# Optimization experiments

Measured on AMD Instinct MI355X. Metric: run time of the kernel, lower is better.

Reference implementation:

```python
import jax, jax.numpy as jnp
import numpy as np

B, C, K, P, STRIDE, ITERS = 32, 32, 3, 4, 1, 3
PSIZE = P * P
EPS = 1e-6


def unfold_patches(x, K, stride):
    # Replicates F.unfold(x_chw, kernel_size=K, padding=K//2, stride=stride)
    # followed by transpose(1,2).view(b, oh, ow, K*K, c) — including the
    # channel-major flat ordering that the view reinterprets.
    b, h, w, c = x.shape
    pad = K // 2
    xp = jnp.pad(jnp.transpose(x, (0, 3, 1, 2)), ((0, 0), (0, 0), (pad, pad), (pad, pad)))
    oh = (h + 2 * pad - K) // stride + 1
    ow = (w + 2 * pad - K) // stride + 1
    rows = []
    for ki in range(K):
        cols = []
        for kj in range(K):
            cols.append(xp[:, :, ki:ki + (oh - 1) * stride + 1:stride, kj:kj + (ow - 1) * stride + 1:stride])
        rows.append(jnp.stack(cols, axis=2))  # (b, c, K, oh, ow)
    pat = jnp.stack(rows, axis=2)  # (b, c, K, K, oh, ow)
    pat = pat.reshape(b, c * K * K, oh * ow)  # unfold output (b, c*K*K, L)
    pat = jnp.transpose(pat, (0, 2, 1)).reshape(b, oh, ow, K * K, c)
    return pat, oh, ow


def squash(s, eps=EPS):
    s2 = jnp.sum(s * s, axis=-1, keepdims=True)
    return (s2 / (1.0 + s2)) * s / jnp.sqrt(s2 + eps)


def dynamic_routing(v, a_in, iters=ITERS, eps=EPS):
    # v: (n, in_votes, C, psize), a_in: (n, in_votes, 1)
    n, in_votes, Cc, _ = v.shape
    b_ij = jnp.zeros((n, in_votes, Cc), dtype=v.dtype)
    a_in = jnp.clip(a_in, 0.0001, 1.0)
    v_j = None
    for t in range(iters):
        c_ij = jax.nn.softmax(b_ij, axis=2) * a_in
        c_ij = c_ij / (jnp.sum(c_ij, axis=2, keepdims=True) + eps)
        s_j = jnp.einsum('nic,nicq->ncq', c_ij, v)
        v_j = squash(s_j)
        if t < iters - 1:
            agreement = jnp.einsum('nicq,ncq->nic', v, v_j)
            b_ij = b_ij + agreement
    a_out = jnp.clip(jnp.sqrt(jnp.sum(v_j * v_j, axis=-1) + eps), 0.0001, 1.0 - 0.0001)
    return v_j, a_out


def setup_inputs() -> dict:
    key = jax.random.key(0)
    k1, k2 = jax.random.split(key)
    x = jax.random.normal(k1, (2, 14, 14, B * (PSIZE + 1)), dtype=jnp.float32)
    weights = jax.random.normal(k2, (K * K * B, C, PSIZE, PSIZE), dtype=jnp.float32) * 0.02
    return {"x": x, "weights": weights}


def reference(x, weights):
    b, h, w, c = x.shape
    patches, oh, ow = unfold_patches(x, K, STRIDE)
    p_in = patches[..., :B * PSIZE].reshape(b * oh * ow, K * K * B, PSIZE)
    a_in = patches[..., B * PSIZE:].reshape(b * oh * ow, K * K * B, 1)
    votes = jnp.einsum('bip,icpq->bicq', p_in, weights)  # (n, KKB, C, psize)
    p_vec, a_vec = dynamic_routing(votes, a_in)
    p_out = p_vec.reshape(b, oh, ow, C * PSIZE)
    a_out = a_vec.reshape(b, oh, ow, C)
    out = jnp.concatenate([p_out, a_out], axis=3)
    p_out = jnp.nan_to_num(p_out, nan=0.0, posinf=10000.0, neginf=-10000.0)
    a_out = jnp.nan_to_num(a_out, nan=0.5, posinf=1.0 - 0.0001, neginf=0.0001)
    out = jnp.nan_to_num(out, nan=0.0, posinf=10000.0, neginf=-10000.0)
    return p_out, a_out, out
```

## Files before the change

### kernel.cpp

```cpp
#include <hip/hip_runtime.h>
#include <hip/hip_fp16.h>
#include <math.h>

#define NB 392
#define NI 288
#define NC 32
#define NQ 16
#define CQ 512
#define CH 544
#define EPSV 1e-6f

#define VSCALE 32.0f
#define VINV (1.0f / 32.0f)

#define OFF_AOUT 200704
#define OFF_CAT  213248

#define RT_THREADS 512
#define RT_WAVES 8

typedef _Float16 v4h __attribute__((ext_vector_type(4)));
typedef float v4f __attribute__((ext_vector_type(4)));
typedef float v2f __attribute__((ext_vector_type(2)));

__device__ __forceinline__ float gather_x(const float* __restrict__ x, int n, int j) {
    int c_idx = j / 9;
    int rem = j - c_idx * 9;
    int ki = rem / 3;
    int kj = rem - ki * 3;
    int b_ = n / 196;
    int rest = n - b_ * 196;
    int yy = rest / 14;
    int xx = rest - yy * 14;
    int iy = yy + ki - 1;
    int ix = xx + kj - 1;
    float v = 0.f;
    if ((unsigned)iy < 14u && (unsigned)ix < 14u)
        v = x[((b_ * 14 + iy) * 14 + ix) * CH + c_idx];
    return v;
}

__global__ __launch_bounds__(256) void votes_k(const float* __restrict__ x,
                                               const float* __restrict__ wts,
                                               uchar* __restrict__ votes) {
    __shared__ ushort w16l[8192];
    __shared__ uchar tile[64 * 144];
    int mtt = blockIdx.x;
    int i = blockIdx.y;
    int t = threadIdx.x;
    int wv = t >> 6;
    int l = t & 63;
    int col = l & 15;
    int quad = l >> 4;

    {
        const float4* src = (const float4*)(wts + (size_t)i * 8192);
#pragma unroll
        for (int it = 0; it < 8; ++it) {
            float4 f4 = src[it * 256 + t];
            int fidx = (it * 256 + t) * 4;
            int c = fidx >> 8;
            int p = (fidx >> 4) & 15;
            int q0 = fidx & 15;
            ushort* wb = &w16l[(c * 16 + q0) * 16 + p];
            wb[0]  = __half_as_ushort(__float2half(f4.x));
            wb[16] = __half_as_ushort(__float2half(f4.y));
            wb[32] = __half_as_ushort(__float2half(f4.z));
            wb[48] = __half_as_ushort(__float2half(f4.w));
        }
    }

    int n_row = mtt * 64 + wv * 16 + col;
    v4h av = {};
    if (n_row < NB) {
        int jb = (i >> 5) * CH + (i & 31) * 16 + quad * 4;
#pragma unroll
        for (int kk = 0; kk < 4; ++kk)
            av[kk] = (_Float16)gather_x(x, n_row, jb + kk);
    }
    __syncthreads();

    for (int ch = 0; ch < 4; ++ch) {
#pragma unroll
        for (int c8 = 0; c8 < 8; ++c8) {
            int ct = ch * 8 + c8;
            v4h bv = *(const v4h*)&w16l[(ct * 16 + col) * 16 + quad * 4];
            v4f acc = {0.f, 0.f, 0.f, 0.f};
            acc = __builtin_amdgcn_mfma_f32_16x16x16f16(av, bv, acc, 0, 0, 0);
            uint u01 = __builtin_amdgcn_cvt_pk_fp8_f32(acc[0] * VSCALE, acc[1] * VSCALE, 0, false);
            uint u23 = __builtin_amdgcn_cvt_pk_fp8_f32(acc[2] * VSCALE, acc[3] * VSCALE, 0, false);
            uchar* tb = &tile[(wv * 16 + quad * 4) * 144 + c8 * 16 + col];
            tb[0 * 144] = (uchar)(u01 & 0xFF);
            tb[1 * 144] = (uchar)((u01 >> 8) & 0xFF);
            tb[2 * 144] = (uchar)(u23 & 0xFF);
            tb[3 * 144] = (uchar)((u23 >> 8) & 0xFF);
        }
        __syncthreads();
#pragma unroll
        for (int k = 0; k < 2; ++k) {
            int idx = k * 256 + t;
            int row = idx >> 3;
            int off = idx & 7;
            int n_out = mtt * 64 + row;
            if (n_out < NB) {
                uint4 d = *(const uint4*)&tile[row * 144 + off * 16];
                *(uint4*)(votes + (((size_t)n_out * NI + i) << 9) + ch * 128 + off * 16) = d;
            }
        }
        __syncthreads();
    }
}

__global__ __launch_bounds__(RT_THREADS) void routing_k(const uchar* __restrict__ votes,
                                                        const float* __restrict__ x,
                                                        float* __restrict__ out) {
    __shared__ float afs[NI];
    __shared__ float sred[RT_WAVES * CQ];
    __shared__ float vj[CQ];
    __shared__ float aout_s[NC];

    int n = blockIdx.x;
    int t = threadIdx.x;
    int wv = t >> 6;
    int l = t & 63;
    int c = l & 31;
    int g = l >> 5;

    if (t < NI) {
        int j = (t >> 5) * CH + 512 + (t & 31);
        float v = gather_x(x, n, j);
        float a = fminf(fmaxf(v, 1e-4f), 1.0f);
        afs[t] = a / (a + EPSV);
    }
    __syncthreads();

    const uchar* vb = votes + (size_t)n * NI * 512;
    float vjr[16];
    float sreg[16];

#define VROW(S) (((const uint4*)(vb + ((size_t)(((((S) << 3) + wv) << 1) + g) << 9)))[c])

    for (int iter = 0; iter < 3; ++iter) {
#pragma unroll
        for (int q = 0; q < 16; ++q) sreg[q] = 0.f;

        uint4 f0 = VROW(0), f1 = VROW(1), f2 = VROW(2);

#pragma clang loop unroll_count(2)
        for (int s = 0; s < 18; ++s) {
            int i = ((s << 3) + wv) * 2 + g;
            uint4 cur = f0;
            f0 = f1; f1 = f2;
            if (s + 3 < 18) f2 = VROW(s + 3);

            float vt[16];
            {
                v2f p;
                p = __builtin_amdgcn_cvt_pk_f32_fp8(cur.x, false); vt[0] = p[0];  vt[1] = p[1];
                p = __builtin_amdgcn_cvt_pk_f32_fp8(cur.x, true);  vt[2] = p[0];  vt[3] = p[1];
                p = __builtin_amdgcn_cvt_pk_f32_fp8(cur.y, false); vt[4] = p[0];  vt[5] = p[1];
                p = __builtin_amdgcn_cvt_pk_f32_fp8(cur.y, true);  vt[6] = p[0];  vt[7] = p[1];
                p = __builtin_amdgcn_cvt_pk_f32_fp8(cur.z, false); vt[8] = p[0];  vt[9] = p[1];
                p = __builtin_amdgcn_cvt_pk_f32_fp8(cur.z, true);  vt[10] = p[0]; vt[11] = p[1];
                p = __builtin_amdgcn_cvt_pk_f32_fp8(cur.w, false); vt[12] = p[0]; vt[13] = p[1];
                p = __builtin_amdgcn_cvt_pk_f32_fp8(cur.w, true);  vt[14] = p[0]; vt[15] = p[1];
            }
            float cij;
            if (iter == 0) {
                cij = afs[i] * (1.0f / 32.0f);
            } else {
                float ah = 0.f;
#pragma unroll
                for (int q = 0; q < 16; ++q) ah += vt[q] * vjr[q];
                float e = __expf(ah);
                float ssum = e;
                ssum += __shfl_xor(ssum, 1);
                ssum += __shfl_xor(ssum, 2);
                ssum += __shfl_xor(ssum, 4);
                ssum += __shfl_xor(ssum, 8);
                ssum += __shfl_xor(ssum, 16);
                cij = e * __builtin_amdgcn_rcpf(ssum) * afs[i];
            }
#pragma unroll
            for (int q = 0; q < 16; ++q) sreg[q] += cij * vt[q];
        }

#pragma unroll
        for (int q = 0; q < 16; ++q) sreg[q] += __shfl_xor(sreg[q], 32);
        if (g == 0) {
            float* sw = &sred[wv * CQ + c];
#pragma unroll
            for (int q = 0; q < 16; ++q) sw[q * 32] = sreg[q];
        }
        __syncthreads();
        {
            float ssum = 0.f;
#pragma unroll
            for (int k = 0; k < RT_WAVES; ++k) ssum += sred[k * CQ + t];
            sred[t] = ssum * VINV;
        }
        __syncthreads();

        if (t < NC) {
            float s2 = 0.f;
#pragma unroll
            for (int q = 0; q < 16; ++q) {
                float s = sred[q * 32 + t];
                s2 += s * s;
            }
            float f = (s2 / (1.f + s2)) / sqrtf(s2 + EPSV);
            float vn2 = 0.f;
#pragma unroll
            for (int q = 0; q < 16; ++q) {
                float v = f * sred[q * 32 + t];
                vj[q * 32 + t] = v;
                vn2 += v * v;
            }
            if (iter == 2) {
                float ao = sqrtf(vn2 + EPSV);
                ao = fminf(fmaxf(ao, 1e-4f), 1.f - 1e-4f);
                aout_s[t] = ao;
            }
        }
        __syncthreads();
        if (iter < 2) {
#pragma unroll
            for (int q = 0; q < 16; ++q) {
                float v = vj[q * 32 + c] * VINV;
                vjr[q] = (iter == 0) ? v : vjr[q] + v;
            }
        }
    }

    {
        float v = vj[(t & 15) * 32 + (t >> 4)];
        out[(size_t)n * CQ + t] = v;
        out[OFF_CAT + (size_t)n * 544 + t] = v;
    }
    if (t < NC) {
        float ao = aout_s[t];
        out[OFF_AOUT + n * 32 + t] = ao;
        out[OFF_CAT + (size_t)n * 544 + 512 + t] = ao;
    }
}

extern "C" void kernel_launch(void* const* d_in, const int* in_sizes, int n_in,
                              void* d_out, int out_size, void* d_ws, size_t ws_size,
                              hipStream_t stream) {
    const float* x = (const float*)d_in[0];
    const float* wts = (const float*)d_in[1];
    float* out = (float*)d_out;
    uchar* votes = (uchar*)d_ws;

    hipLaunchKernelGGL(votes_k, dim3(7, NI), dim3(256), 0, stream,
                       x, wts, votes);
    hipLaunchKernelGGL(routing_k, dim3(NB), dim3(RT_THREADS), 0, stream,
                       votes, x, out);
}
```

Before: 120.4 us.

## Pre-convert weights to transposed fp16 in a separate kernel

Adds a prep kernel that converts the weights to fp16 once, already in the transposed layout the MFMA B operand needs, and writes them to workspace. The votes kernel then reads B fragments directly from global memory and drops its shared-memory weight staging and one barrier. Before, each of the 7 row-tile blocks per capsule re-read and re-converted the same fp32 weights. The cost is an extra kernel launch, an extra global round trip for the weights, and uncoalesced 8-byte global loads inside the MFMA loop.

```diff
diff --git a/kernel.cpp b/kernel.cpp
--- a/kernel.cpp
+++ b/kernel.cpp
@@ -12,6 +12,8 @@
 
 #define VSCALE 32.0f
 #define VINV (1.0f / 32.0f)
+
+#define VOT_BYTES ((size_t)NB * NI * 512)
 
 #define OFF_AOUT 200704
 #define OFF_CAT  213248
@@ -40,10 +42,38 @@
     return v;
 }
 
+__global__ __launch_bounds__(256) void prep_w(const float* __restrict__ wts,
+                                              ushort* __restrict__ w16) {
+    __shared__ float wl[4096];
+    int i = blockIdx.x >> 1;
+    int h = blockIdx.x & 1;
+    int t = threadIdx.x;
+    const float4* src = (const float4*)(wts + (size_t)i * 8192 + h * 4096);
+#pragma unroll
+    for (int it = 0; it < 4; ++it)
+        *(float4*)&wl[(it * 256 + t) * 4] = src[it * 256 + t];
+    __syncthreads();
+    uint4* dst = (uint4*)(w16 + (size_t)i * 8192 + h * 4096);
+#pragma unroll
+    for (int it = 0; it < 2; ++it) {
+        int idx = it * 256 + t;
+        int cl = idx >> 1;
+        int m = idx & 1;
+        int base = (cl >> 4) * 256 + (cl & 15);
+        uint v[4];
+#pragma unroll
+        for (int kk = 0; kk < 4; ++kk) {
+            __half2 hh = __floats2half2_rn(wl[base + (8 * m + 2 * kk) * 16],
+                                           wl[base + (8 * m + 2 * kk + 1) * 16]);
+            v[kk] = *(uint*)&hh;
+        }
+        dst[cl * 2 + m] = make_uint4(v[0], v[1], v[2], v[3]);
+    }
+}
+
 __global__ __launch_bounds__(256) void votes_k(const float* __restrict__ x,
-                                               const float* __restrict__ wts,
+                                               const ushort* __restrict__ w16,
                                                uchar* __restrict__ votes) {
-    __shared__ ushort w16l[8192];
     __shared__ uchar tile[64 * 144];
     int mtt = blockIdx.x;
     int i = blockIdx.y;
@@ -53,23 +83,6 @@
     int col = l & 15;
     int quad = l >> 4;
 
-    {
-        const float4* src = (const float4*)(wts + (size_t)i * 8192);
-#pragma unroll
-        for (int it = 0; it < 8; ++it) {
-            float4 f4 = src[it * 256 + t];
-            int fidx = (it * 256 + t) * 4;
-            int c = fidx >> 8;
-            int p = (fidx >> 4) & 15;
-            int q0 = fidx & 15;
-            ushort* wb = &w16l[(c * 16 + q0) * 16 + p];
-            wb[0]  = __half_as_ushort(__float2half(f4.x));
-            wb[16] = __half_as_ushort(__float2half(f4.y));
-            wb[32] = __half_as_ushort(__float2half(f4.z));
-            wb[48] = __half_as_ushort(__float2half(f4.w));
-        }
-    }
-
     int n_row = mtt * 64 + wv * 16 + col;
     v4h av = {};
     if (n_row < NB) {
@@ -78,13 +91,14 @@
         for (int kk = 0; kk < 4; ++kk)
             av[kk] = (_Float16)gather_x(x, n_row, jb + kk);
     }
-    __syncthreads();
+
+    const ushort* wbase = w16 + (size_t)i * 8192;
 
     for (int ch = 0; ch < 4; ++ch) {
 #pragma unroll
         for (int c8 = 0; c8 < 8; ++c8) {
             int ct = ch * 8 + c8;
-            v4h bv = *(const v4h*)&w16l[(ct * 16 + col) * 16 + quad * 4];
+            v4h bv = *(const v4h*)(wbase + (ct * 16 + col) * 16 + quad * 4);
             v4f acc = {0.f, 0.f, 0.f, 0.f};
             acc = __builtin_amdgcn_mfma_f32_16x16x16f16(av, bv, acc, 0, 0, 0);
             uint u01 = __builtin_amdgcn_cvt_pk_fp8_f32(acc[0] * VSCALE, acc[1] * VSCALE, 0, false);
@@ -251,9 +265,11 @@
     const float* wts = (const float*)d_in[1];
     float* out = (float*)d_out;
     uchar* votes = (uchar*)d_ws;
-
+    ushort* w16 = (ushort*)((uchar*)d_ws + VOT_BYTES);
+
+    hipLaunchKernelGGL(prep_w, dim3(NI * 2), dim3(256), 0, stream, wts, w16);
     hipLaunchKernelGGL(votes_k, dim3(7, NI), dim3(256), 0, stream,
-                       x, wts, votes);
+                       x, w16, votes);
     hipLaunchKernelGGL(routing_k, dim3(NB), dim3(RT_THREADS), 0, stream,
                        votes, x, out);
 }
```

Result: faster. 116.9 us (-3.0%).
